# Performance work log

Measured on AMD Instinct MI355X. Metric: run time of the kernel, lower is better.

The kernel has to match this reference:

```python
import jax, jax.numpy as jnp
import numpy as np

EPS = 1e-8
SIGMA_MIN = 1e-4
B, T, C, P = 32, 8192, 64, 168


def setup_inputs() -> dict:
    key = jax.random.key(0)
    k1, k2, k3, k4, k5 = jax.random.split(key, 5)
    x_full = jax.random.normal(k1, (B, T, C), dtype=jnp.float32)
    mask = (jax.random.uniform(k2, (B, T, C)) > 0.2).astype(jnp.float32)
    x = mask * x_full  # observed input with missing positions zeroed
    phase_id = jax.random.randint(k3, (B,), 0, P, dtype=jnp.int64)
    anchor_mu = jax.random.normal(k4, (P, C), dtype=jnp.float32)
    anchor_log_sigma = 0.1 * jax.random.normal(k5, (P, C), dtype=jnp.float32)
    return {
        "x": x,
        "mask": mask,
        "phase_id": phase_id,
        "anchor_mu": anchor_mu,
        "anchor_log_sigma": anchor_log_sigma,
        "tau0_raw": jnp.zeros((1,), dtype=jnp.float32),
        "tau1_raw": jnp.zeros((1,), dtype=jnp.float32),
        "missing_token": jnp.zeros((1, 1, C), dtype=jnp.float32),
    }


def _max_gap_ratio(mask):
    # longest contiguous missing run (channel 0) as fraction of T -> (B,1,1)
    missing = mask[:, :, 0] < 0.5  # (B, T)
    Tlen = missing.shape[1]
    idx = jnp.arange(Tlen)[None, :]  # (1, T)
    # index of most recent observed position (running max), -1 if none yet
    last_obs = jax.lax.associative_scan(jnp.maximum,
                                        jnp.where(missing, -1, idx), axis=1)
    run = jnp.where(missing, idx - last_obs, 0)  # current missing run length
    max_run = run.max(axis=1).astype(jnp.float32)
    return (max_run / Tlen)[:, None, None]


def reference(x, mask, phase_id, anchor_mu, anchor_log_sigma,
              tau0_raw, tau1_raw, missing_token):
    # masked moments over time axis
    mask_sum = jnp.clip(mask.sum(axis=1, keepdims=True), EPS, None)  # (B,1,C)
    mu_obs = (mask * x).sum(axis=1, keepdims=True) / mask_sum
    var_obs = (mask * (x - mu_obs) ** 2).sum(axis=1, keepdims=True) / mask_sum
    sigma_obs = jnp.sqrt(var_obs + EPS)

    # anchor lookup
    mu_ref = anchor_mu[phase_id][:, None, :]              # (B,1,C)
    log_sigma_ref = anchor_log_sigma[phase_id][:, None, :]

    coverage = mask.mean(axis=1, keepdims=True)           # (B,1,C)
    gap_ratio = _max_gap_ratio(mask)                      # (B,1,1)

    tau0 = jax.nn.softplus(tau0_raw)
    tau1 = jax.nn.softplus(tau1_raw)
    w = coverage / (coverage + tau0 + tau1 * gap_ratio + EPS)

    mu = w * mu_obs + (1.0 - w) * mu_ref
    log_sigma = w * jnp.log(sigma_obs + EPS) + (1.0 - w) * log_sigma_ref
    sigma = jnp.clip(jnp.exp(log_sigma), SIGMA_MIN, None)

    z = (x - mu) / sigma
    return mask * z + (1.0 - mask) * missing_token
```

## Files before the change

kernel.cpp:

```cpp
#include <hip/hip_runtime.h>
#include <math.h>

#define B_ 32
#define T_ 8192
#define C_ 64
#define S_ 32
#define L_ (T_ / S_)
#define EPS_ 1e-8f
#define SIGMA_MIN_ 1e-4f

#define SUM_OFF 0
#define SQ_OFF  65536
#define MS_OFF  131072
#define GAP_OFF 196608
#define MU_OFF  200704
#define INV_OFF 202752

__global__ __launch_bounds__(256) void k1_stats(const float* __restrict__ x,
                                                const float* __restrict__ mask,
                                                float* __restrict__ ws) {
    const int bid = blockIdx.x;
    const int b   = bid / S_;
    const int s   = bid % S_;
    const int tid = threadIdx.x;
    const int cq  = tid & 15;
    const int tg  = tid >> 4;

    const float4* x4 = (const float4*)x;
    const float4* m4 = (const float4*)mask;
    const long base = (long)(b * T_ + s * L_) * 16 + cq;

    float4 s1 = make_float4(0.f, 0.f, 0.f, 0.f);
    float4 s2 = make_float4(0.f, 0.f, 0.f, 0.f);
    float4 sm = make_float4(0.f, 0.f, 0.f, 0.f);

#pragma unroll
    for (int it = 0; it < L_ / 16; ++it) {
        long idx = base + (long)(it * 16 + tg) * 16;
        float4 xv = x4[idx];
        float4 mv = m4[idx];
        s1.x += xv.x; s1.y += xv.y; s1.z += xv.z; s1.w += xv.w;
        s2.x += xv.x * xv.x; s2.y += xv.y * xv.y;
        s2.z += xv.z * xv.z; s2.w += xv.w * xv.w;
        sm.x += mv.x; sm.y += mv.y; sm.z += mv.z; sm.w += mv.w;
    }

    __shared__ float4 shA[256];
    __shared__ float4 shB[256];
    __shared__ float4 shC[256];
    shA[tid] = s1; shB[tid] = s2; shC[tid] = sm;
    __syncthreads();

    for (int off = 128; off >= 16; off >>= 1) {
        if (tid < off) {
            float4 a = shA[tid], b2 = shA[tid + off];
            a.x += b2.x; a.y += b2.y; a.z += b2.z; a.w += b2.w; shA[tid] = a;
            float4 c = shB[tid], d = shB[tid + off];
            c.x += d.x; c.y += d.y; c.z += d.z; c.w += d.w; shB[tid] = c;
            float4 e = shC[tid], f = shC[tid + off];
            e.x += f.x; e.y += f.y; e.z += f.z; e.w += f.w; shC[tid] = e;
        }
        __syncthreads();
    }

    if (tid < 16) {
        const int o = bid * C_ + tid * 4;
        ((float4*)(ws + SUM_OFF))[o >> 2] = shA[tid];
        ((float4*)(ws + SQ_OFF ))[o >> 2] = shB[tid];
        ((float4*)(ws + MS_OFF ))[o >> 2] = shC[tid];
    }

    const int t = s * L_ + tid;
    const float m0 = mask[((long)b * T_ + t) * C_];
    const bool miss = (m0 < 0.5f);
    unsigned long long w = __ballot(miss);

    __shared__ unsigned long long words[4];
    if ((tid & 63) == 0) words[tid >> 6] = w;
    __syncthreads();

    if (tid == 0) {
        int pre = 0, suf = 0, best = 0, len = 0;
        for (int i = 0; i < 4; ++i) {
            unsigned long long wi = words[i];
            int p_i, s_i, b_i;
            if (wi == ~0ull) {
                p_i = 64; s_i = 64; b_i = 64;
            } else {
                p_i = __builtin_ctzll(~wi);
                s_i = __builtin_clzll(~wi);
                unsigned long long tmp = wi; b_i = 0;
                while (tmp) { tmp &= (tmp << 1); ++b_i; }
            }
            if (i == 0) { pre = p_i; suf = s_i; best = b_i; len = 64; }
            else {
                int cross = suf + p_i;
                best = max(best, max(b_i, cross));
                pre  = (pre == len) ? len + p_i : pre;
                suf  = (s_i == 64) ? suf + 64 : s_i;
                len += 64;
            }
        }
        int* gp = (int*)(ws + GAP_OFF) + bid * 4;
        gp[0] = pre; gp[1] = suf; gp[2] = best;
    }
}

__global__ __launch_bounds__(64) void k2_params(const int*   __restrict__ phase_id,
                                                const float* __restrict__ anchor_mu,
                                                const float* __restrict__ anchor_ls,
                                                const float* __restrict__ tau0_raw,
                                                const float* __restrict__ tau1_raw,
                                                float* __restrict__ ws) {
    const int b = blockIdx.x;
    const int c = threadIdx.x;

    __shared__ float sh_gap;
    if (c == 0) {
        const int* gp = (const int*)(ws + GAP_OFF);
        int pre = 0, suf = 0, best = 0, len = 0;
        for (int s = 0; s < S_; ++s) {
            const int* g = gp + (b * S_ + s) * 4;
            int p_i = g[0], s_i = g[1], b_i = g[2];
            if (s == 0) { pre = p_i; suf = s_i; best = b_i; len = L_; }
            else {
                int cross = suf + p_i;
                best = max(best, max(b_i, cross));
                pre  = (pre == len) ? len + p_i : pre;
                suf  = (s_i == L_) ? suf + L_ : s_i;
                len += L_;
            }
        }
        sh_gap = (float)best / (float)T_;
    }
    __syncthreads();

    float sum = 0.f, sq = 0.f, ms = 0.f;
    for (int s = 0; s < S_; ++s) {
        int o = (b * S_ + s) * C_ + c;
        sum += ws[SUM_OFF + o];
        sq  += ws[SQ_OFF  + o];
        ms  += ws[MS_OFF  + o];
    }

    const float msc    = fmaxf(ms, EPS_);
    const float mu_obs = sum / msc;
    float var = (sq - 2.f * mu_obs * sum + mu_obs * mu_obs * ms) / msc;
    var = fmaxf(var, 0.f);
    const float sigma_obs = sqrtf(var + EPS_);
    const float coverage  = ms / (float)T_;

    const float t0 = log1pf(expf(tau0_raw[0]));
    const float t1 = log1pf(expf(tau1_raw[0]));
    const float w  = coverage / (coverage + t0 + t1 * sh_gap + EPS_);

    const int   pid    = phase_id[b];
    const float mu_ref = anchor_mu[pid * C_ + c];
    const float ls_ref = anchor_ls[pid * C_ + c];

    const float mu = w * mu_obs + (1.f - w) * mu_ref;
    const float ls = w * logf(sigma_obs + EPS_) + (1.f - w) * ls_ref;
    const float sigma = fmaxf(expf(ls), SIGMA_MIN_);

    ws[MU_OFF  + b * C_ + c] = mu;
    ws[INV_OFF + b * C_ + c] = 1.f / sigma;
}

__global__ __launch_bounds__(256) void k3_norm(const float* __restrict__ x,
                                               const float* __restrict__ mask,
                                               const float* __restrict__ token,
                                               const float* __restrict__ ws,
                                               float* __restrict__ out) {
    const int gid = blockIdx.x * 256 + threadIdx.x;
    const float4* x4 = (const float4*)x;
    const float4* m4 = (const float4*)mask;
    const float4* mu4  = (const float4*)(ws + MU_OFF);
    const float4* inv4 = (const float4*)(ws + INV_OFF);
    const float4* tk4  = (const float4*)token;

    const int b = gid >> 17;
    const int p = b * 16 + (gid & 15);

    float4 xv = x4[gid];
    float4 mv = m4[gid];
    float4 mu = mu4[p];
    float4 iv = inv4[p];
    float4 tk = tk4[gid & 15];

    float4 o;
    o.x = mv.x * ((xv.x - mu.x) * iv.x) + (1.f - mv.x) * tk.x;
    o.y = mv.y * ((xv.y - mu.y) * iv.y) + (1.f - mv.y) * tk.y;
    o.z = mv.z * ((xv.z - mu.z) * iv.z) + (1.f - mv.z) * tk.z;
    o.w = mv.w * ((xv.w - mu.w) * iv.w) + (1.f - mv.w) * tk.w;

    ((float4*)out)[gid] = o;
}

extern "C" void kernel_launch(void* const* d_in, const int* in_sizes, int n_in,
                              void* d_out, int out_size, void* d_ws, size_t ws_size,
                              hipStream_t stream) {
    const float* x    = (const float*)d_in[0];
    const float* mask = (const float*)d_in[1];
    const int*   pid  = (const int*)  d_in[2];
    const float* amu  = (const float*)d_in[3];
    const float* als  = (const float*)d_in[4];
    const float* t0   = (const float*)d_in[5];
    const float* t1   = (const float*)d_in[6];
    const float* tok  = (const float*)d_in[7];
    float* out = (float*)d_out;
    float* ws  = (float*)d_ws;

    k1_stats<<<B_ * S_, 256, 0, stream>>>(x, mask, ws);
    k2_params<<<B_, 64, 0, stream>>>(pid, amu, als, t0, t1, ws);
    const int n4 = B_ * T_ * C_ / 4;
    k3_norm<<<n4 / 256, 256, 0, stream>>>(x, mask, tok, ws, out);
}
```

Measured before the change: 61.17 us.

## Split stats pass into more blocks with shuffle reductions and parallel param reduce

```diff
diff --git a/kernel.cpp b/kernel.cpp
--- a/kernel.cpp
+++ b/kernel.cpp
@@ -4,124 +4,122 @@
 #define B_ 32
 #define T_ 8192
 #define C_ 64
-#define S_ 32
+#define S_ 128
 #define L_ (T_ / S_)
 #define EPS_ 1e-8f
 #define SIGMA_MIN_ 1e-4f
 
 #define SUM_OFF 0
-#define SQ_OFF  65536
-#define MS_OFF  131072
-#define GAP_OFF 196608
-#define MU_OFF  200704
-#define INV_OFF 202752
+#define SQ_OFF  262144
+#define MS_OFF  524288
+#define GAP_OFF 786432
+#define MU_OFF  802816
+#define INV_OFF 804864
+
+__device__ inline float4 f4add(float4 a, float4 b) {
+    return make_float4(a.x + b.x, a.y + b.y, a.z + b.z, a.w + b.w);
+}
+__device__ inline float4 f4shfl_xor(float4 v, int m) {
+    float4 r;
+    r.x = __shfl_xor(v.x, m);
+    r.y = __shfl_xor(v.y, m);
+    r.z = __shfl_xor(v.z, m);
+    r.w = __shfl_xor(v.w, m);
+    return r;
+}
 
 __global__ __launch_bounds__(256) void k1_stats(const float* __restrict__ x,
                                                 const float* __restrict__ mask,
                                                 float* __restrict__ ws) {
     const int bid = blockIdx.x;
-    const int b   = bid / S_;
-    const int s   = bid % S_;
+    const int b   = bid >> 7;
+    const int s   = bid & (S_ - 1);
     const int tid = threadIdx.x;
     const int cq  = tid & 15;
-    const int tg  = tid >> 4;
+    const int row = (tid >> 4) & 3;
+    const int wv  = tid >> 6;
 
     const float4* x4 = (const float4*)x;
     const float4* m4 = (const float4*)mask;
-    const long base = (long)(b * T_ + s * L_) * 16 + cq;
+    const long base = ((long)b * T_ + (long)s * L_) * 16 + cq;
+
+    float4 xv[4], mv[4];
+#pragma unroll
+    for (int it = 0; it < 4; ++it) {
+        long idx = base + (long)(it * 16 + wv * 4 + row) * 16;
+        xv[it] = x4[idx];
+        mv[it] = m4[idx];
+    }
 
     float4 s1 = make_float4(0.f, 0.f, 0.f, 0.f);
     float4 s2 = make_float4(0.f, 0.f, 0.f, 0.f);
     float4 sm = make_float4(0.f, 0.f, 0.f, 0.f);
-
 #pragma unroll
-    for (int it = 0; it < L_ / 16; ++it) {
-        long idx = base + (long)(it * 16 + tg) * 16;
-        float4 xv = x4[idx];
-        float4 mv = m4[idx];
-        s1.x += xv.x; s1.y += xv.y; s1.z += xv.z; s1.w += xv.w;
-        s2.x += xv.x * xv.x; s2.y += xv.y * xv.y;
-        s2.z += xv.z * xv.z; s2.w += xv.w * xv.w;
-        sm.x += mv.x; sm.y += mv.y; sm.z += mv.z; sm.w += mv.w;
-    }
-
-    __shared__ float4 shA[256];
-    __shared__ float4 shB[256];
-    __shared__ float4 shC[256];
-    shA[tid] = s1; shB[tid] = s2; shC[tid] = sm;
+    for (int it = 0; it < 4; ++it) {
+        s1.x += xv[it].x; s1.y += xv[it].y; s1.z += xv[it].z; s1.w += xv[it].w;
+        s2.x += xv[it].x * xv[it].x; s2.y += xv[it].y * xv[it].y;
+        s2.z += xv[it].z * xv[it].z; s2.w += xv[it].w * xv[it].w;
+        sm.x += mv[it].x; sm.y += mv[it].y; sm.z += mv[it].z; sm.w += mv[it].w;
+    }
+
+    s1 = f4add(s1, f4shfl_xor(s1, 16)); s1 = f4add(s1, f4shfl_xor(s1, 32));
+    s2 = f4add(s2, f4shfl_xor(s2, 16)); s2 = f4add(s2, f4shfl_xor(s2, 32));
+    sm = f4add(sm, f4shfl_xor(sm, 16)); sm = f4add(sm, f4shfl_xor(sm, 32));
+
+    __shared__ float4 shA[4][16];
+    __shared__ float4 shB[4][16];
+    __shared__ float4 shC[4][16];
+    if ((tid & 63) < 16) { shA[wv][cq] = s1; shB[wv][cq] = s2; shC[wv][cq] = sm; }
     __syncthreads();
 
-    for (int off = 128; off >= 16; off >>= 1) {
-        if (tid < off) {
-            float4 a = shA[tid], b2 = shA[tid + off];
-            a.x += b2.x; a.y += b2.y; a.z += b2.z; a.w += b2.w; shA[tid] = a;
-            float4 c = shB[tid], d = shB[tid + off];
-            c.x += d.x; c.y += d.y; c.z += d.z; c.w += d.w; shB[tid] = c;
-            float4 e = shC[tid], f = shC[tid + off];
-            e.x += f.x; e.y += f.y; e.z += f.z; e.w += f.w; shC[tid] = e;
+    if (tid < 16) {
+        float4 a = f4add(f4add(shA[0][tid], shA[1][tid]), f4add(shA[2][tid], shA[3][tid]));
+        float4 c = f4add(f4add(shB[0][tid], shB[1][tid]), f4add(shB[2][tid], shB[3][tid]));
+        float4 e = f4add(f4add(shC[0][tid], shC[1][tid]), f4add(shC[2][tid], shC[3][tid]));
+        const int o = (bid * C_ + tid * 4) >> 2;
+        ((float4*)(ws + SUM_OFF))[o] = a;
+        ((float4*)(ws + SQ_OFF ))[o] = c;
+        ((float4*)(ws + MS_OFF ))[o] = e;
+    }
+
+    if (tid < 64) {
+        const float m0 = mask[((long)b * T_ + (long)s * L_ + tid) * C_];
+        unsigned long long bal = __ballot(m0 < 0.5f);
+        if (tid == 0) {
+            int pre, suf, best;
+            if (bal == ~0ull) {
+                pre = 64; suf = 64; best = 64;
+            } else {
+                pre = __builtin_ctzll(~bal);
+                suf = __builtin_clzll(~bal);
+                unsigned long long tmp = bal; best = 0;
+                while (tmp) { tmp &= (tmp << 1); ++best; }
+            }
+            int* gp = (int*)(ws + GAP_OFF) + bid * 4;
+            gp[0] = pre; gp[1] = suf; gp[2] = best;
         }
-        __syncthreads();
-    }
-
-    if (tid < 16) {
-        const int o = bid * C_ + tid * 4;
-        ((float4*)(ws + SUM_OFF))[o >> 2] = shA[tid];
-        ((float4*)(ws + SQ_OFF ))[o >> 2] = shB[tid];
-        ((float4*)(ws + MS_OFF ))[o >> 2] = shC[tid];
-    }
-
-    const int t = s * L_ + tid;
-    const float m0 = mask[((long)b * T_ + t) * C_];
-    const bool miss = (m0 < 0.5f);
-    unsigned long long w = __ballot(miss);
-
-    __shared__ unsigned long long words[4];
-    if ((tid & 63) == 0) words[tid >> 6] = w;
-    __syncthreads();
+    }
+}
+
+__global__ __launch_bounds__(256) void k2_params(const int*   __restrict__ phase_id,
+                                                 const float* __restrict__ anchor_mu,
+                                                 const float* __restrict__ anchor_ls,
+                                                 const float* __restrict__ tau0_raw,
+                                                 const float* __restrict__ tau1_raw,
+                                                 float* __restrict__ ws) {
+    const int b   = blockIdx.x;
+    const int tid = threadIdx.x;
+    const int c   = tid & 63;
+    const int p   = tid >> 6;
+
+    __shared__ float sh_gap;
+    __shared__ float sh[3][4][64];
 
     if (tid == 0) {
-        int pre = 0, suf = 0, best = 0, len = 0;
-        for (int i = 0; i < 4; ++i) {
-            unsigned long long wi = words[i];
-            int p_i, s_i, b_i;
-            if (wi == ~0ull) {
-                p_i = 64; s_i = 64; b_i = 64;
-            } else {
-                p_i = __builtin_ctzll(~wi);
-                s_i = __builtin_clzll(~wi);
-                unsigned long long tmp = wi; b_i = 0;
-                while (tmp) { tmp &= (tmp << 1); ++b_i; }
-            }
-            if (i == 0) { pre = p_i; suf = s_i; best = b_i; len = 64; }
-            else {
-                int cross = suf + p_i;
-                best = max(best, max(b_i, cross));
-                pre  = (pre == len) ? len + p_i : pre;
-                suf  = (s_i == 64) ? suf + 64 : s_i;
-                len += 64;
-            }
-        }
-        int* gp = (int*)(ws + GAP_OFF) + bid * 4;
-        gp[0] = pre; gp[1] = suf; gp[2] = best;
-    }
-}
-
-__global__ __launch_bounds__(64) void k2_params(const int*   __restrict__ phase_id,
-                                                const float* __restrict__ anchor_mu,
-                                                const float* __restrict__ anchor_ls,
-                                                const float* __restrict__ tau0_raw,
-                                                const float* __restrict__ tau1_raw,
-                                                float* __restrict__ ws) {
-    const int b = blockIdx.x;
-    const int c = threadIdx.x;
-
-    __shared__ float sh_gap;
-    if (c == 0) {
-        const int* gp = (const int*)(ws + GAP_OFF);
+        const int* gp = (const int*)(ws + GAP_OFF) + b * S_ * 4;
         int pre = 0, suf = 0, best = 0, len = 0;
         for (int s = 0; s < S_; ++s) {
-            const int* g = gp + (b * S_ + s) * 4;
-            int p_i = g[0], s_i = g[1], b_i = g[2];
+            int p_i = gp[s * 4], s_i = gp[s * 4 + 1], b_i = gp[s * 4 + 2];
             if (s == 0) { pre = p_i; suf = s_i; best = b_i; len = L_; }
             else {
                 int cross = suf + p_i;
@@ -133,37 +131,44 @@
         }
         sh_gap = (float)best / (float)T_;
     }
-    __syncthreads();
 
     float sum = 0.f, sq = 0.f, ms = 0.f;
-    for (int s = 0; s < S_; ++s) {
+    for (int s = p; s < S_; s += 4) {
         int o = (b * S_ + s) * C_ + c;
         sum += ws[SUM_OFF + o];
         sq  += ws[SQ_OFF  + o];
         ms  += ws[MS_OFF  + o];
     }
-
-    const float msc    = fmaxf(ms, EPS_);
-    const float mu_obs = sum / msc;
-    float var = (sq - 2.f * mu_obs * sum + mu_obs * mu_obs * ms) / msc;
-    var = fmaxf(var, 0.f);
-    const float sigma_obs = sqrtf(var + EPS_);
-    const float coverage  = ms / (float)T_;
-
-    const float t0 = log1pf(expf(tau0_raw[0]));
-    const float t1 = log1pf(expf(tau1_raw[0]));
-    const float w  = coverage / (coverage + t0 + t1 * sh_gap + EPS_);
-
-    const int   pid    = phase_id[b];
-    const float mu_ref = anchor_mu[pid * C_ + c];
-    const float ls_ref = anchor_ls[pid * C_ + c];
-
-    const float mu = w * mu_obs + (1.f - w) * mu_ref;
-    const float ls = w * logf(sigma_obs + EPS_) + (1.f - w) * ls_ref;
-    const float sigma = fmaxf(expf(ls), SIGMA_MIN_);
-
-    ws[MU_OFF  + b * C_ + c] = mu;
-    ws[INV_OFF + b * C_ + c] = 1.f / sigma;
+    sh[0][p][c] = sum; sh[1][p][c] = sq; sh[2][p][c] = ms;
+    __syncthreads();
+
+    if (tid < 64) {
+        sum = sh[0][0][c] + sh[0][1][c] + sh[0][2][c] + sh[0][3][c];
+        sq  = sh[1][0][c] + sh[1][1][c] + sh[1][2][c] + sh[1][3][c];
+        ms  = sh[2][0][c] + sh[2][1][c] + sh[2][2][c] + sh[2][3][c];
+
+        const float msc    = fmaxf(ms, EPS_);
+        const float mu_obs = sum / msc;
+        float var = (sq - 2.f * mu_obs * sum + mu_obs * mu_obs * ms) / msc;
+        var = fmaxf(var, 0.f);
+        const float sigma_obs = sqrtf(var + EPS_);
+        const float coverage  = ms / (float)T_;
+
+        const float t0 = log1pf(expf(tau0_raw[0]));
+        const float t1 = log1pf(expf(tau1_raw[0]));
+        const float w  = coverage / (coverage + t0 + t1 * sh_gap + EPS_);
+
+        const int   pid    = phase_id[b];
+        const float mu_ref = anchor_mu[pid * C_ + c];
+        const float ls_ref = anchor_ls[pid * C_ + c];
+
+        const float mu = w * mu_obs + (1.f - w) * mu_ref;
+        const float ls = w * logf(sigma_obs + EPS_) + (1.f - w) * ls_ref;
+        const float sigma = fmaxf(expf(ls), SIGMA_MIN_);
+
+        ws[MU_OFF  + b * C_ + c] = mu;
+        ws[INV_OFF + b * C_ + c] = 1.f / sigma;
+    }
 }
 
 __global__ __launch_bounds__(256) void k3_norm(const float* __restrict__ x,
@@ -211,7 +216,7 @@
     float* ws  = (float*)d_ws;
 
     k1_stats<<<B_ * S_, 256, 0, stream>>>(x, mask, ws);
-    k2_params<<<B_, 64, 0, stream>>>(pid, amu, als, t0, t1, ws);
+    k2_params<<<B_, 256, 0, stream>>>(pid, amu, als, t0, t1, ws);
     const int n4 = B_ * T_ * C_ / 4;
     k3_norm<<<n4 / 256, 256, 0, stream>>>(x, mask, tok, ws, out);
 }
```

Result: slower. 75.20 us (+22.9%).
